# Kernel optimization log

Hardware: AMD Instinct MI355X
Metric: run time of the kernel (lower is better)

## Reference

```python
import jax, jax.numpy as jnp
import numpy as np

N = 50000      # nodes / stations
E = 600000     # edges
IN = 16        # in_channels
ED = 8         # edge_dim
HID = 128      # hidden
H = 4          # heads
C = HID // H   # 32 per-head channels
EMB = HID // 2 # station embedding dim
FEAT = HID - EMB
SLOPE = 0.2    # GATv2 LeakyReLU negative slope


def setup_inputs() -> dict:
    key = jax.random.key(0)
    ks = jax.random.split(key, 32)
    r = lambda i, shape, s=0.05: (jax.random.normal(ks[i], shape, jnp.float32) * s)
    inp = {
        "x": jax.random.normal(ks[0], (N, IN), jnp.float32),
        "node_idx": jax.random.randint(ks[1], (N,), 0, N),
        "edge_index": jax.random.randint(ks[2], (2, E), 0, N),
        "edge_attr": jax.random.normal(ks[3], (E, ED), jnp.float32),
        # params
        "emb": r(4, (N, EMB)),
        "W_in": r(5, (IN, FEAT)), "b_in": jnp.zeros((FEAT,), jnp.float32),
        # conv1 (GATv2: lin_l, lin_r, lin_edge, att, out bias)
        "Wl1": r(6, (HID, HID)), "bl1": jnp.zeros((HID,), jnp.float32),
        "Wr1": r(7, (HID, HID)), "br1": jnp.zeros((HID,), jnp.float32),
        "We1": r(8, (ED, HID)),  "be1": jnp.zeros((HID,), jnp.float32),
        "att1": r(9, (H, C)),    "bo1": jnp.zeros((HID,), jnp.float32),
        # conv2
        "Wl2": r(10, (HID, HID)), "bl2": jnp.zeros((HID,), jnp.float32),
        "Wr2": r(11, (HID, HID)), "br2": jnp.zeros((HID,), jnp.float32),
        "We2": r(12, (ED, HID)),  "be2": jnp.zeros((HID,), jnp.float32),
        "att2": r(13, (H, C)),    "bo2": jnp.zeros((HID,), jnp.float32),
        # layer norms
        "g1": jnp.ones((HID,), jnp.float32), "beta1": jnp.zeros((HID,), jnp.float32),
        "g2": jnp.ones((HID,), jnp.float32), "beta2": jnp.zeros((HID,), jnp.float32),
        # output head
        "W_out": r(14, (HID, 1)), "b_out": jnp.zeros((1,), jnp.float32),
    }
    return inp


def _gatv2(x, src, dst, ea, Wl, bl, Wr, br, We, be, att, bo):
    # x: [N,HID] -> per-head projections [N,H,C]
    xl = (x @ Wl + bl).reshape(-1, H, C)   # source transform
    xr = (x @ Wr + br).reshape(-1, H, C)   # target transform
    ee = (ea @ We + be).reshape(-1, H, C)  # edge transform [E,H,C]
    s = jax.nn.leaky_relu(xl[src] + xr[dst] + ee, SLOPE)  # [E,H,C]
    logit = jnp.einsum('ehc,hc->eh', s, att)              # [E,H]
    # segment softmax over destination node
    amax = jax.lax.stop_gradient(jax.ops.segment_max(logit, dst, num_segments=N))
    amax = jnp.where(jnp.isfinite(amax), amax, 0.0)
    ex = jnp.exp(logit - amax[dst])
    den = jax.ops.segment_sum(ex, dst, num_segments=N)
    alpha = ex / den[dst]                                  # [E,H]
    out = jax.ops.segment_sum(xl[src] * alpha[..., None], dst, num_segments=N)
    return out.reshape(-1, HID) + bo


def _ln(x, g, b):
    mu = x.mean(-1, keepdims=True)
    v = ((x - mu) ** 2).mean(-1, keepdims=True)
    return (x - mu) * jax.lax.rsqrt(v + 1e-5) * g + b


def reference(x, node_idx, edge_index, edge_attr, emb, W_in, b_in,
              Wl1, bl1, Wr1, br1, We1, be1, att1, bo1,
              Wl2, bl2, Wr2, br2, We2, be2, att2, bo2,
              g1, beta1, g2, beta2, W_out, b_out):
    src, dst = edge_index[0], edge_index[1]
    feat = jax.nn.relu(x @ W_in + b_in)                       # [N,FEAT]
    z = jnp.concatenate([feat, emb[node_idx]], axis=-1)       # [N,HID]
    h = jax.nn.relu(_gatv2(z, src, dst, edge_attr, Wl1, bl1, Wr1, br1, We1, be1, att1, bo1))
    z = _ln(z + h, g1, beta1)
    h = jax.nn.relu(_gatv2(z, src, dst, edge_attr, Wl2, bl2, Wr2, br2, We2, be2, att2, bo2))
    z = _ln(z + h, g2, beta2)
    return (z @ W_out + b_out).squeeze(-1)                    # [N]
```

## Files before the change

kernel.cpp:

```cpp
#include <hip/hip_runtime.h>
#include <hip/hip_bf16.h>

#define NN 50000
#define NE 600000
#define IND 16
#define EDD 8
#define HIDD 128
#define NH 4
#define CC 32
#define EMBD 64
#define FEATD 64
#define NB_SCAN ((NN + 255) / 256)

typedef __hip_bfloat16 bf16;
typedef __attribute__((ext_vector_type(8))) short bshort8;
typedef __attribute__((ext_vector_type(4))) float floatx4;
typedef __attribute__((ext_vector_type(2))) float f32x2;

__device__ __forceinline__ unsigned short f2bu(float f) {
    unsigned int u = __float_as_uint(f);
    u += 0x7fffu + ((u >> 16) & 1u);
    return (unsigned short)(u >> 16);
}

#if defined(__has_builtin)
#if __has_builtin(__builtin_amdgcn_fdot2_f32_bf16)
#define HAS_DOT2BF 1
#endif
#endif
#ifndef HAS_DOT2BF
#define HAS_DOT2BF 0
#endif

#if HAS_DOT2BF
typedef __attribute__((ext_vector_type(2))) __bf16 bfx2;
__device__ __forceinline__ float dot2bf(unsigned int a, unsigned int b, float c) {
    return __builtin_amdgcn_fdot2_f32_bf16(__builtin_bit_cast(bfx2, a),
                                           __builtin_bit_cast(bfx2, b), c, false);
}
#else
__device__ __forceinline__ float dot2bf(unsigned int a, unsigned int b, float c) {
    float a0 = __uint_as_float(a << 16), a1 = __uint_as_float(a & 0xffff0000u);
    float b0 = __uint_as_float(b << 16), b1 = __uint_as_float(b & 0xffff0000u);
    return __builtin_fmaf(a1, b1, __builtin_fmaf(a0, b0, c));
}
#endif

template <bool F32>
__device__ __forceinline__ float LD(const void* p, long long i) {
    if constexpr (F32) return ((const float*)p)[i];
    else return __bfloat162float(((const bf16*)p)[i]);
}

__device__ __forceinline__ bool is_f32(const int* cnt) { return *cnt > 8; }

__global__ void k_detinit(const unsigned short* __restrict__ x, int nhalf,
                          int* __restrict__ cnt, int* __restrict__ deg,
                          int* __restrict__ dcnt) {
    if (blockIdx.x == 0) {
        __shared__ int red[256];
        int hits = 0;
        for (int i = threadIdx.x; i < nhalf; i += 256)
            if ((x[i] & 0x7F80u) == 0x7F80u) hits++;
        red[threadIdx.x] = hits;
        __syncthreads();
        for (int o = 128; o; o >>= 1) {
            if (threadIdx.x < o) red[threadIdx.x] += red[threadIdx.x + o];
            __syncthreads();
        }
        if (threadIdx.x == 0) *cnt = red[0];
    } else {
        int gid = (blockIdx.x - 1) * 256 + threadIdx.x;
        if (gid < NN) deg[gid] = 0;
        if (blockIdx.x == 1 && threadIdx.x < 64) dcnt[threadIdx.x] = 0;
    }
}

__global__ void k_hist(const int* __restrict__ ei, int* __restrict__ deg, int* __restrict__ rank) {
    int e = blockIdx.x * blockDim.x + threadIdx.x;
    if (e < NE) rank[e] = atomicAdd(&deg[ei[NE + e]], 1);
}

__global__ void k_scan1(const int* __restrict__ deg, int* __restrict__ off,
                        int* __restrict__ bsum, int* __restrict__ dcnt,
                        int* __restrict__ rankd) {
    __shared__ int tile[256];
    __shared__ int lh[64];
    __shared__ int lbase[64];
    int t = threadIdx.x;
    int gid = blockIdx.x * 256 + t;
    if (t < 64) lh[t] = 0;
    __syncthreads();
    int v = (gid < NN) ? deg[gid] : 0;
    int b = min(v, 63);
    int lr = 0;
    if (gid < NN) lr = atomicAdd(&lh[b], 1);
    tile[t] = v;
    __syncthreads();
    if (t < 64) lbase[t] = lh[t] ? atomicAdd(&dcnt[t], lh[t]) : 0;
    #pragma unroll
    for (int o = 1; o < 256; o <<= 1) {
        int u = (t >= o) ? tile[t - o] : 0;
        __syncthreads();
        tile[t] += u;
        __syncthreads();
    }
    if (gid < NN) {
        off[gid] = tile[t] - v;
        rankd[gid] = lbase[b] + lr;
    }
    if (t == 255) bsum[blockIdx.x] = tile[255];
}
__global__ void k_scan2(int* __restrict__ bsum, int* __restrict__ dcnt,
                        int* __restrict__ dbase) {
    __shared__ int tile[256];
    __shared__ int d2[64];
    int t = threadIdx.x;
    int v = (t < NB_SCAN) ? bsum[t] : 0;
    tile[t] = v;
    int dv = (t < 64) ? dcnt[t] : 0;
    if (t < 64) d2[t] = dv;
    __syncthreads();
    #pragma unroll
    for (int o = 1; o < 256; o <<= 1) {
        int u = (t >= o) ? tile[t - o] : 0;
        __syncthreads();
        tile[t] += u;
        __syncthreads();
    }
    #pragma unroll
    for (int o = 1; o < 64; o <<= 1) {
        int u = (t >= o && t < 64) ? d2[t - o] : 0;
        __syncthreads();
        if (t < 64) d2[t] += u;
        __syncthreads();
    }
    if (t < NB_SCAN) bsum[t] = tile[t] - v;
    if (t < 64) dbase[t] = d2[t] - dv;
}
__global__ void k_scan3(int* __restrict__ off, const int* __restrict__ bsum,
                        const int* __restrict__ deg, const int* __restrict__ rankd,
                        const int* __restrict__ dbase, int* __restrict__ perm) {
    int gid = blockIdx.x * 256 + threadIdx.x;
    if (gid < NN) {
        off[gid] += bsum[blockIdx.x];
        int b = min(deg[gid], 63);
        perm[dbase[b] + rankd[gid]] = gid;
    }
    if (gid == 0) off[NN] = NE;
}

template <bool F32>
__device__ void fill_impl(const int* __restrict__ ei, const int* __restrict__ off,
                          const int* __restrict__ rank, int* __restrict__ esrc,
                          uint4* __restrict__ ea8, const void* ea) {
    int e = blockIdx.x * blockDim.x + threadIdx.x;
    if (e >= NE) return;
    if (e < 6) {
        esrc[NE + e] = 0;
        uint4 z; z.x = 0; z.y = 0; z.z = 0; z.w = 0;
        ea8[NE + e] = z;
    }
    int slot = off[ei[NE + e]] + rank[e];
    esrc[slot] = ei[e];
    unsigned int w[4];
    #pragma unroll
    for (int d = 0; d < 4; d++) {
        unsigned int lo = f2bu(LD<F32>(ea, (long long)e * EDD + 2 * d));
        unsigned int hi = f2bu(LD<F32>(ea, (long long)e * EDD + 2 * d + 1));
        w[d] = lo | (hi << 16);
    }
    uint4 v; v.x = w[0]; v.y = w[1]; v.z = w[2]; v.w = w[3];
    ea8[slot] = v;
}
__global__ void k_fill(const int* cnt, const int* ei, const int* off, const int* rank,
                       int* esrc, uint4* ea8, const void* ea) {
    if (is_f32(cnt)) fill_impl<true>(ei, off, rank, esrc, ea8, ea);
    else             fill_impl<false>(ei, off, rank, esrc, ea8, ea);
}

template <bool F32>
__device__ void bzpw_impl(const void* x, const int* __restrict__ node_idx, const void* emb,
                          const void* W_in, const void* b_in, bf16* __restrict__ zb,
                          const void* Wl1, const void* bl1, const void* Wr1, const void* br1,
                          const void* Wl2, const void* bl2, const void* Wr2, const void* br2,
                          bf16* __restrict__ wbT, float* __restrict__ bias) {
    int t = threadIdx.x;
    if (blockIdx.x < NN) {
        int n = blockIdx.x;
        float val;
        if (t < FEATD) {
            float acc = LD<F32>(b_in, t);
            #pragma unroll
            for (int k = 0; k < IND; k++)
                acc += LD<F32>(x, (long long)n * IND + k) * LD<F32>(W_in, k * FEATD + t);
            val = fmaxf(acc, 0.f);
        } else {
            val = LD<F32>(emb, (long long)node_idx[n] * EMBD + (t - FEATD));
        }
        zb[n * HIDD + t] = __float2bfloat16(val);
    } else {
        int bid = blockIdx.x - NN;
        int layer = bid >> 8;
        int n = bid & 255;
        const void* W = layer ? (n < HIDD ? Wl2 : Wr2) : (n < HIDD ? Wl1 : Wr1);
        const void* b = layer ? (n < HIDD ? bl2 : br2) : (n < HIDD ? bl1 : br1);
        int nn = n & (HIDD - 1);
        wbT[(layer * 256 + n) * HIDD + t] = __float2bfloat16(LD<F32>(W, t * HIDD + nn));
        if (t == 0) bias[layer * 256 + n] = LD<F32>(b, nn);
    }
}
__global__ void k_bzpw(const int* cnt, const void* x, const int* node_idx, const void* emb,
                       const void* W_in, const void* b_in, bf16* zb,
                       const void* Wl1, const void* bl1, const void* Wr1, const void* br1,
                       const void* Wl2, const void* bl2, const void* Wr2, const void* br2,
                       bf16* wbT, float* bias) {
    if (is_f32(cnt)) bzpw_impl<true>(x, node_idx, emb, W_in, b_in, zb, Wl1, bl1, Wr1, br1,
                                     Wl2, bl2, Wr2, br2, wbT, bias);
    else             bzpw_impl<false>(x, node_idx, emb, W_in, b_in, zb, Wl1, bl1, Wr1, br1,
                                      Wl2, bl2, Wr2, br2, wbT, bias);
}

__global__ __launch_bounds__(256) void k_projmm(const bf16* __restrict__ zb,
                                                const bf16* __restrict__ wbT,
                                                const float* __restrict__ bias,
                                                bf16* __restrict__ xl, bf16* __restrict__ xr) {
    int wave = threadIdx.x >> 6, lane = threadIdx.x & 63;
    int m0 = blockIdx.x * 32;
    int n0 = wave * 64;
    int l15 = lane & 15, q = lane >> 4;
    bshort8 bfr[4][4];
    #pragma unroll
    for (int j = 0; j < 4; j++)
        #pragma unroll
        for (int s = 0; s < 4; s++)
            bfr[j][s] = *(const bshort8*)(wbT + ((n0 + j * 16 + l15) << 7) + s * 32 + q * 8);
    float bv[4];
    #pragma unroll
    for (int j = 0; j < 4; j++) bv[j] = bias[n0 + j * 16 + l15];
    const bf16* arow0 = zb + ((m0 + l15) << 7) + q * 8;
    const bf16* arow1 = arow0 + (16 << 7);
    bshort8 a0[4], a1[4];
    #pragma unroll
    for (int s = 0; s < 4; s++) a0[s] = *(const bshort8*)(arow0 + s * 32);
    #pragma unroll
    for (int s = 0; s < 4; s++) a1[s] = *(const bshort8*)(arow1 + s * 32);
    #pragma unroll
    for (int mi = 0; mi < 2; mi++) {
        floatx4 acc0 = {0.f, 0.f, 0.f, 0.f}, acc1 = acc0, acc2 = acc0, acc3 = acc0;
        #pragma unroll
        for (int s = 0; s < 4; s++) {
            bshort8 a = mi ? a1[s] : a0[s];
            acc0 = __builtin_amdgcn_mfma_f32_16x16x32_bf16(a, bfr[0][s], acc0, 0, 0, 0);
            acc1 = __builtin_amdgcn_mfma_f32_16x16x32_bf16(a, bfr[1][s], acc1, 0, 0, 0);
            acc2 = __builtin_amdgcn_mfma_f32_16x16x32_bf16(a, bfr[2][s], acc2, 0, 0, 0);
            acc3 = __builtin_amdgcn_mfma_f32_16x16x32_bf16(a, bfr[3][s], acc3, 0, 0, 0);
        }
        floatx4 accs[4] = {acc0, acc1, acc2, acc3};
        #pragma unroll
        for (int j = 0; j < 4; j++) {
            int colg = n0 + j * 16 + l15;
            bf16* dst = (colg < HIDD) ? (xl + colg) : (xr + (colg - HIDD));
            #pragma unroll
            for (int r = 0; r < 4; r++) {
                int rowc = m0 + mi * 16 + q * 4 + r;
                if (rowc < NN) dst[rowc << 7] = __float2bfloat16(accs[j][r] + bv[j]);
            }
        }
    }
}

__device__ __forceinline__ void edge_body(uint4 eu, uint2 xu, const unsigned int (*wp)[4],
                                          const float* base, const f32x2* at2,
                                          float mask, f32x2* acc, float& den) {
    f32x2 xv0, xv1;
    xv0.x = __uint_as_float(xu.x << 16); xv0.y = __uint_as_float(xu.x & 0xffff0000u);
    xv1.x = __uint_as_float(xu.y << 16); xv1.y = __uint_as_float(xu.y & 0xffff0000u);
    f32x2 e01, e23;
    {
        float c0 = base[0];
        c0 = dot2bf(eu.x, wp[0][0], c0);
        c0 = dot2bf(eu.y, wp[1][0], c0);
        c0 = dot2bf(eu.z, wp[2][0], c0);
        c0 = dot2bf(eu.w, wp[3][0], c0);
        float c1 = base[1];
        c1 = dot2bf(eu.x, wp[0][1], c1);
        c1 = dot2bf(eu.y, wp[1][1], c1);
        c1 = dot2bf(eu.z, wp[2][1], c1);
        c1 = dot2bf(eu.w, wp[3][1], c1);
        e01.x = c0; e01.y = c1;
        float c2 = base[2];
        c2 = dot2bf(eu.x, wp[0][2], c2);
        c2 = dot2bf(eu.y, wp[1][2], c2);
        c2 = dot2bf(eu.z, wp[2][2], c2);
        c2 = dot2bf(eu.w, wp[3][2], c2);
        float c3 = base[3];
        c3 = dot2bf(eu.x, wp[0][3], c3);
        c3 = dot2bf(eu.y, wp[1][3], c3);
        c3 = dot2bf(eu.z, wp[2][3], c3);
        c3 = dot2bf(eu.w, wp[3][3], c3);
        e23.x = c2; e23.y = c3;
    }
    f32x2 s0 = xv0 + e01;
    f32x2 s1 = xv1 + e23;
    s0 = __builtin_elementwise_max(s0, s0 * 0.2f);
    s1 = __builtin_elementwise_max(s1, s1 * 0.2f);
    f32x2 lsv = s0 * at2[0] + s1 * at2[1];
    float ls = lsv.x + lsv.y;
    ls += __shfl_xor(ls, 1);
    ls += __shfl_xor(ls, 2);
    ls += __shfl_xor(ls, 4);
    float ex = exp2f(ls) * mask;
    acc[0] += ex * xv0;
    acc[1] += ex * xv1;
    den += ex;
}

template <bool F32, bool LAST>
__device__ void gat_impl(const int* __restrict__ perm,
                         const int* __restrict__ off, const int* __restrict__ esrc,
                         const uint4* __restrict__ ea8,
                         const void* We, const void* be, const void* att,
                         const bf16* __restrict__ xl, const bf16* __restrict__ xr,
                         const void* bo, bf16* __restrict__ zb,
                         const void* g, const void* beta,
                         const void* Wo, const void* bout, void* out) {
    int wave = threadIdx.x >> 6;
    int half = (threadIdx.x >> 5) & 1;
    int lane5 = threadIdx.x & 31;
    int n = perm[blockIdx.x * 8 + wave * 2 + half];
    int c0 = lane5 << 2;
    unsigned int wp[4][4];
    #pragma unroll
    for (int p = 0; p < 4; p++)
        #pragma unroll
        for (int j = 0; j < 4; j++) {
            unsigned int lo = f2bu(LD<F32>(We, (2 * p) * HIDD + c0 + j));
            unsigned int hi = f2bu(LD<F32>(We, (2 * p + 1) * HIDD + c0 + j));
            wp[p][j] = lo | (hi << 16);
        }
    const float L2E = 1.4426950408889634f;
    f32x2 at2[2];
    at2[0].x = LD<F32>(att, c0 + 0) * L2E;
    at2[0].y = LD<F32>(att, c0 + 1) * L2E;
    at2[1].x = LD<F32>(att, c0 + 2) * L2E;
    at2[1].y = LD<F32>(att, c0 + 3) * L2E;
    uint2 xru = *(const uint2*)(xr + (n << 7) + c0);
    float xrv[4];
    xrv[0] = __uint_as_float(xru.x << 16);
    xrv[1] = __uint_as_float(xru.x & 0xffff0000u);
    xrv[2] = __uint_as_float(xru.y << 16);
    xrv[3] = __uint_as_float(xru.y & 0xffff0000u);
    float base[4];
    #pragma unroll
    for (int j = 0; j < 4; j++) base[j] = LD<F32>(be, c0 + j) + xrv[j];
    int lo = off[n], hi = off[n + 1];
    f32x2 accA[2] = {{0.f, 0.f}, {0.f, 0.f}}, accB[2] = {{0.f, 0.f}, {0.f, 0.f}};
    float denA = 0.f, denB = 0.f;
    if (lo < hi) {
        int sA = esrc[lo],      sB = esrc[lo + 1];
        uint4 eA = ea8[lo],     eB = ea8[lo + 1];
        uint2 xA = *(const uint2*)(xl + (sA << 7) + c0);
        uint2 xB = *(const uint2*)(xl + (sB << 7) + c0);
        int snA = esrc[lo + 2], snB = esrc[lo + 3];
        uint4 enA = ea8[lo + 2], enB = ea8[lo + 3];
        for (int i = lo; i < hi; i += 2) {
            uint2 xnA = *(const uint2*)(xl + (snA << 7) + c0);
            uint2 xnB = *(const uint2*)(xl + (snB << 7) + c0);
            int s2A = esrc[i + 4],  s2B = esrc[i + 5];
            uint4 e2A = ea8[i + 4], e2B = ea8[i + 5];
            edge_body(eA, xA, wp, base, at2, 1.f, accA, denA);
            float mB = (i + 1 < hi) ? 1.f : 0.f;
            edge_body(eB, xB, wp, base, at2, mB, accB, denB);
            eA = enA; eB = enB; xA = xnA; xB = xnB;
            snA = s2A; snB = s2B; enA = e2A; enB = e2B;
        }
        accA[0] += accB[0];
        accA[1] += accB[1];
        denA += denB;
    }
    float inv = (denA > 0.f) ? 1.0f / denA : 0.f;
    uint2 zu = *(const uint2*)(zb + (n << 7) + c0);
    float zv[4];
    zv[0] = __uint_as_float(zu.x << 16);
    zv[1] = __uint_as_float(zu.x & 0xffff0000u);
    zv[2] = __uint_as_float(zu.y << 16);
    zv[3] = __uint_as_float(zu.y & 0xffff0000u);
    float accf[4] = {accA[0].x, accA[0].y, accA[1].x, accA[1].y};
    float v[4];
    float s = 0.f;
    #pragma unroll
    for (int j = 0; j < 4; j++) {
        float hv = fmaxf(accf[j] * inv + LD<F32>(bo, c0 + j), 0.f);
        v[j] = zv[j] + hv;
        s += v[j];
    }
    #pragma unroll
    for (int m = 16; m; m >>= 1) s += __shfl_xor(s, m);
    float mu = s * (1.f / HIDD);
    float s2 = 0.f;
    float dv[4];
    #pragma unroll
    for (int j = 0; j < 4; j++) { dv[j] = v[j] - mu; s2 += dv[j] * dv[j]; }
    #pragma unroll
    for (int m = 16; m; m >>= 1) s2 += __shfl_xor(s2, m);
    float rs = rsqrtf(s2 * (1.f / HIDD) + 1e-5f);
    float o[4];
    #pragma unroll
    for (int j = 0; j < 4; j++)
        o[j] = dv[j] * rs * LD<F32>(g, c0 + j) + LD<F32>(beta, c0 + j);
    if constexpr (!LAST) {
        uint2 pk;
        pk.x = (unsigned int)f2bu(o[0]) | ((unsigned int)f2bu(o[1]) << 16);
        pk.y = (unsigned int)f2bu(o[2]) | ((unsigned int)f2bu(o[3]) << 16);
        *(uint2*)(zb + (n << 7) + c0) = pk;
    } else {
        float po = 0.f;
        #pragma unroll
        for (int j = 0; j < 4; j++) po += o[j] * LD<F32>(Wo, c0 + j);
        #pragma unroll
        for (int m = 16; m; m >>= 1) po += __shfl_xor(po, m);
        if (lane5 == 0) {
            float r = po + LD<F32>(bout, 0);
            if constexpr (F32) ((float*)out)[n] = r;
            else               ((bf16*)out)[n] = __float2bfloat16(r);
        }
    }
}
__global__ void k_gat(const int* cnt, const int* perm, const int* off, const int* esrc,
                      const uint4* ea8, const void* We, const void* be, const void* att,
                      const bf16* xl, const bf16* xr, const void* bo, bf16* zb,
                      const void* g, const void* beta) {
    if (is_f32(cnt)) gat_impl<true, false>(perm, off, esrc, ea8, We, be, att, xl, xr, bo, zb, g, beta, nullptr, nullptr, nullptr);
    else             gat_impl<false, false>(perm, off, esrc, ea8, We, be, att, xl, xr, bo, zb, g, beta, nullptr, nullptr, nullptr);
}
__global__ void k_gat_last(const int* cnt, const int* perm, const int* off, const int* esrc,
                           const uint4* ea8, const void* We, const void* be, const void* att,
                           const bf16* xl, const bf16* xr, const void* bo, bf16* zb,
                           const void* g, const void* beta,
                           const void* Wo, const void* bout, void* out) {
    if (is_f32(cnt)) gat_impl<true, true>(perm, off, esrc, ea8, We, be, att, xl, xr, bo, zb, g, beta, Wo, bout, out);
    else             gat_impl<false, true>(perm, off, esrc, ea8, We, be, att, xl, xr, bo, zb, g, beta, Wo, bout, out);
}

extern "C" void kernel_launch(void* const* d_in, const int* in_sizes, int n_in,
                              void* d_out, int out_size, void* d_ws, size_t ws_size,
                              hipStream_t stream) {
    const void* x        = d_in[0];
    const int*  node_idx = (const int*)d_in[1];
    const int*  ei       = (const int*)d_in[2];
    const void* ea       = d_in[3];
    const void* emb      = d_in[4];
    const void* W_in     = d_in[5];
    const void* b_in     = d_in[6];
    const void* Wl1 = d_in[7];  const void* bl1 = d_in[8];
    const void* Wr1 = d_in[9];  const void* br1 = d_in[10];
    const void* We1 = d_in[11]; const void* be1 = d_in[12];
    const void* att1 = d_in[13]; const void* bo1 = d_in[14];
    const void* Wl2 = d_in[15]; const void* bl2 = d_in[16];
    const void* Wr2 = d_in[17]; const void* br2 = d_in[18];
    const void* We2 = d_in[19]; const void* be2 = d_in[20];
    const void* att2 = d_in[21]; const void* bo2 = d_in[22];
    const void* g1 = d_in[23]; const void* beta1 = d_in[24];
    const void* g2 = d_in[25]; const void* beta2 = d_in[26];
    const void* W_out = d_in[27]; const void* b_out = d_in[28];

    int*   cnt   = (int*)d_ws;
    uint4* ea8   = (uint4*)((char*)d_ws + 256);
    bf16*  zb    = (bf16*)(ea8 + NE + 8);
    bf16*  xl    = zb + NN * HIDD;
    bf16*  xr    = xl + NN * HIDD;
    bf16*  wbT   = xr + NN * HIDD;
    float* bias  = (float*)(wbT + 2 * 256 * HIDD);
    int*   off   = (int*)(bias + 512);
    int*   deg   = off + NN + 1;
    int*   rank  = deg + NN;
    int*   rankd = rank + NE;
    int*   perm  = rankd + NN;
    int*   esrc  = perm + NN;
    int*   bsum  = esrc + NE + 8;
    int*   dcnt  = bsum + 256;
    int*   dbase = dcnt + 64;

    int nhalf = in_sizes[0] < 16384 ? in_sizes[0] : 16384;
    k_detinit<<<NB_SCAN + 1, 256, 0, stream>>>((const unsigned short*)x, nhalf, cnt, deg, dcnt);
    k_hist<<<(NE + 255) / 256, 256, 0, stream>>>(ei, deg, rank);
    k_scan1<<<NB_SCAN, 256, 0, stream>>>(deg, off, bsum, dcnt, rankd);
    k_scan2<<<1, 256, 0, stream>>>(bsum, dcnt, dbase);
    k_scan3<<<NB_SCAN, 256, 0, stream>>>(off, bsum, deg, rankd, dbase, perm);
    k_bzpw<<<NN + 512, HIDD, 0, stream>>>(cnt, x, node_idx, emb, W_in, b_in, zb,
                                          Wl1, bl1, Wr1, br1, Wl2, bl2, Wr2, br2, wbT, bias);
    k_fill<<<(NE + 255) / 256, 256, 0, stream>>>(cnt, ei, off, rank, esrc, ea8, ea);

    k_projmm<<<(NN + 31) / 32, 256, 0, stream>>>(zb, wbT, bias, xl, xr);
    k_gat<<<NN / 8, 256, 0, stream>>>(cnt, perm, off, esrc, ea8, We1, be1, att1, xl, xr, bo1, zb, g1, beta1);

    k_projmm<<<(NN + 31) / 32, 256, 0, stream>>>(zb, wbT + 256 * HIDD, bias + 256, xl, xr);
    k_gat_last<<<NN / 8, 256, 0, stream>>>(cnt, perm, off, esrc, ea8, We2, be2, att2, xl, xr, bo2, zb,
                                           g2, beta2, W_out, b_out, d_out);
}
```

Measured before the change: 385.2 us.

## Deepen gather prefetch pipeline, sort nodes by descending degree, vectorize edge fill

The GATv2 edge loop now software-pipelines one more stage, prefetching source indices and edge attributes three pairs ahead and gathered xl rows two pairs ahead, to hide more gather latency. The degree-bucket permutation is reversed so high-degree nodes are scheduled first, which should reduce tail imbalance. The fill kernel loads edge attributes as float4 pairs, or copies bf16 inputs directly, instead of doing scalar loads. The tail padding grows to 8 entries to cover the deeper prefetch, and register pressure rises.

```diff
diff --git a/kernel.cpp b/kernel.cpp
--- a/kernel.cpp
+++ b/kernel.cpp
@@ -92,7 +92,7 @@
     if (t < 64) lh[t] = 0;
     __syncthreads();
     int v = (gid < NN) ? deg[gid] : 0;
-    int b = min(v, 63);
+    int b = 63 - min(v, 63);
     int lr = 0;
     if (gid < NN) lr = atomicAdd(&lh[b], 1);
     tile[t] = v;
@@ -144,7 +144,7 @@
     int gid = blockIdx.x * 256 + threadIdx.x;
     if (gid < NN) {
         off[gid] += bsum[blockIdx.x];
-        int b = min(deg[gid], 63);
+        int b = 63 - min(deg[gid], 63);
         perm[dbase[b] + rankd[gid]] = gid;
     }
     if (gid == 0) off[NN] = NE;
@@ -156,21 +156,24 @@
                           uint4* __restrict__ ea8, const void* ea) {
     int e = blockIdx.x * blockDim.x + threadIdx.x;
     if (e >= NE) return;
-    if (e < 6) {
+    if (e < 8) {
         esrc[NE + e] = 0;
         uint4 z; z.x = 0; z.y = 0; z.z = 0; z.w = 0;
         ea8[NE + e] = z;
     }
     int slot = off[ei[NE + e]] + rank[e];
     esrc[slot] = ei[e];
-    unsigned int w[4];
-    #pragma unroll
-    for (int d = 0; d < 4; d++) {
-        unsigned int lo = f2bu(LD<F32>(ea, (long long)e * EDD + 2 * d));
-        unsigned int hi = f2bu(LD<F32>(ea, (long long)e * EDD + 2 * d + 1));
-        w[d] = lo | (hi << 16);
-    }
-    uint4 v; v.x = w[0]; v.y = w[1]; v.z = w[2]; v.w = w[3];
+    uint4 v;
+    if constexpr (F32) {
+        const float4* ef = (const float4*)ea;
+        float4 f0 = ef[2 * e], f1 = ef[2 * e + 1];
+        v.x = (unsigned int)f2bu(f0.x) | ((unsigned int)f2bu(f0.y) << 16);
+        v.y = (unsigned int)f2bu(f0.z) | ((unsigned int)f2bu(f0.w) << 16);
+        v.z = (unsigned int)f2bu(f1.x) | ((unsigned int)f2bu(f1.y) << 16);
+        v.w = (unsigned int)f2bu(f1.z) | ((unsigned int)f2bu(f1.w) << 16);
+    } else {
+        v = ((const uint4*)ea)[e];
+    }
     ea8[slot] = v;
 }
 __global__ void k_fill(const int* cnt, const int* ei, const int* off, const int* rank,
@@ -360,20 +363,27 @@
     if (lo < hi) {
         int sA = esrc[lo],      sB = esrc[lo + 1];
         uint4 eA = ea8[lo],     eB = ea8[lo + 1];
+        int snA = esrc[lo + 2], snB = esrc[lo + 3];
+        uint4 enA = ea8[lo + 2], enB = ea8[lo + 3];
+        int s2A = esrc[lo + 4], s2B = esrc[lo + 5];
+        uint4 e2A = ea8[lo + 4], e2B = ea8[lo + 5];
         uint2 xA = *(const uint2*)(xl + (sA << 7) + c0);
         uint2 xB = *(const uint2*)(xl + (sB << 7) + c0);
-        int snA = esrc[lo + 2], snB = esrc[lo + 3];
-        uint4 enA = ea8[lo + 2], enB = ea8[lo + 3];
+        uint2 xnA = *(const uint2*)(xl + (snA << 7) + c0);
+        uint2 xnB = *(const uint2*)(xl + (snB << 7) + c0);
         for (int i = lo; i < hi; i += 2) {
-            uint2 xnA = *(const uint2*)(xl + (snA << 7) + c0);
-            uint2 xnB = *(const uint2*)(xl + (snB << 7) + c0);
-            int s2A = esrc[i + 4],  s2B = esrc[i + 5];
-            uint4 e2A = ea8[i + 4], e2B = ea8[i + 5];
+            uint2 x2A = *(const uint2*)(xl + (s2A << 7) + c0);
+            uint2 x2B = *(const uint2*)(xl + (s2B << 7) + c0);
+            int s3A = esrc[i + 6],  s3B = esrc[i + 7];
+            uint4 e3A = ea8[i + 6], e3B = ea8[i + 7];
             edge_body(eA, xA, wp, base, at2, 1.f, accA, denA);
             float mB = (i + 1 < hi) ? 1.f : 0.f;
             edge_body(eB, xB, wp, base, at2, mB, accB, denB);
-            eA = enA; eB = enB; xA = xnA; xB = xnB;
-            snA = s2A; snB = s2B; enA = e2A; enB = e2B;
+            eA = enA; enA = e2A; e2A = e3A;
+            eB = enB; enB = e2B; e2B = e3B;
+            xA = xnA; xnA = x2A;
+            xB = xnB; xnB = x2B;
+            s2A = s3A; s2B = s3B;
         }
         accA[0] += accB[0];
         accA[1] += accB[1];
```

After: 365.9 us. 1.05x faster.
